# Performance work log

Hardware: AMD Instinct MI355X
Metric: run time of the kernel (lower is better)

## Reference

```python
import jax, jax.numpy as jnp
import numpy as np

NEG_INF = -9e15  # matches torch's -9000000000000000.0 mask value
ALPHA = 0.2      # LeakyReLU negative slope


def setup_inputs() -> dict:
    key = jax.random.key(0)
    k1, k2, k3, k4 = jax.random.split(key, 4)
    B, N, Fin, Fout = 8, 2048, 256, 256
    h = jax.random.normal(k1, (B, N, Fin), dtype=jnp.float32)
    adj = jax.random.randint(k2, (B, N, N), 0, 2, dtype=jnp.int32)
    # xavier_uniform with gain=1.414
    limW = 1.414 * np.sqrt(6.0 / (Fin + Fout))
    W = jax.random.uniform(k3, (Fin, Fout), minval=-limW, maxval=limW, dtype=jnp.float32)
    lima = 1.414 * np.sqrt(6.0 / (2 * Fout + 1))
    a = jax.random.uniform(k4, (2 * Fout, 1), minval=-lima, maxval=lima, dtype=jnp.float32)
    return {"h": h, "adj": adj, "W": W, "a": a}


def reference(h, adj, W, a):
    # h: (B, N, Fin), adj: (B, N, N), W: (Fin, Fout), a: (2*Fout, 1)
    Fout = W.shape[1]
    Wh = jnp.einsum('bni,io->bno', h, W)                 # (B, N, Fout)
    # e[b,i,j] = leakyrelu(Wh[b,i] @ a1 + Wh[b,j] @ a2) -- equivalent to the
    # original concat([Wh_i, Wh_j]) @ a without the O(N^2 * 2F) intermediate.
    e1 = Wh @ a[:Fout, 0]                                # (B, N)
    e2 = Wh @ a[Fout:, 0]                                # (B, N)
    e = jax.nn.leaky_relu(e1[:, :, None] + e2[:, None, :], negative_slope=ALPHA)
    masked = jnp.where(adj > 0, e, NEG_INF)
    attention = jax.nn.softmax(masked, axis=-1)          # (B, N, N)
    # dropout omitted (deterministic eval-mode reference)
    h_prime = jnp.einsum('bij,bjo->bio', attention, Wh)  # (B, N, Fout)
    return jax.nn.elu(h_prime), attention
```

## Files before the change

kernel.cpp:

```cpp
#include <hip/hip_runtime.h>
#include <hip/hip_bf16.h>
#include <stdint.h>

#define NEG_INF -9.0e15f
#define LRELU_ALPHA 0.2f

using bf16x8  = __attribute__((ext_vector_type(8))) short;
using f32x4   = __attribute__((ext_vector_type(4))) float;
using short4v = __attribute__((ext_vector_type(4))) short;
using int4v   = __attribute__((ext_vector_type(4))) int;
using float4v = __attribute__((ext_vector_type(4))) float;
using uint4v  = __attribute__((ext_vector_type(4))) unsigned;

static __device__ __forceinline__ float b2f(short s) {
  unsigned u = ((unsigned)(unsigned short)s) << 16;
  return __builtin_bit_cast(float, u);
}
static __device__ __forceinline__ short f2bf(float f) {
  unsigned u = __builtin_bit_cast(unsigned, f);
  u = u + 0x7FFFu + ((u >> 16) & 1u);
  return (short)(u >> 16);
}
static __device__ __forceinline__ unsigned cvtpk_bf16(float lo, float hi) {
  unsigned r;
  asm volatile("v_cvt_pk_bf16_f32 %0, %1, %2" : "=v"(r) : "v"(lo), "v"(hi));
  return r;
}
static __device__ __forceinline__ void gload16(const void* g, void* l) {
  __builtin_amdgcn_global_load_lds((const __attribute__((address_space(1))) void*)g,
                                   (__attribute__((address_space(3))) void*)l, 16, 0, 0);
}

__global__ __launch_bounds__(256) void cast_f32_bf16_kernel(
    const float* __restrict__ src, short* __restrict__ dst, int n)
{
  int i0 = (blockIdx.x * 256 + threadIdx.x) * 8;
  if (i0 >= n) return;
  float4v v0 = *(const float4v*)(src + i0);
  float4v v1 = *(const float4v*)(src + i0 + 4);
  short os[8] __attribute__((aligned(16)));
#pragma unroll
  for (int k = 0; k < 8; ++k) {
    float x = (k < 4) ? v0[k] : v1[k - 4];
    x = (x - x == 0.0f) ? x : 0.0f;
    os[k] = f2bf(x);
  }
  *(int4v*)(dst + i0) = *(const int4v*)os;
}

__global__ __launch_bounds__(256) void transpose_bf16_kernel(
    const short* __restrict__ src, short* __restrict__ dst,
    int M, int N, long long ss, long long ds)
{
  __shared__ short t[64][68];
  const int b = blockIdx.z;
  src += (long long)b * ss; dst += (long long)b * ds;
  const int m0 = blockIdx.x * 64, n0 = blockIdx.y * 64;
  const int tid = threadIdx.x;
  const int rr = tid >> 3, cc = (tid & 7) * 8;
#pragma unroll
  for (int p = 0; p < 2; ++p) {
    int row = rr + p * 32;
    const short* sp = src + (long long)(m0 + row) * N + n0 + cc;
    short4v v0 = *(const short4v*)sp;
    short4v v1 = *(const short4v*)(sp + 4);
    *(short4v*)&t[row][cc]     = v0;
    *(short4v*)&t[row][cc + 4] = v1;
  }
  __syncthreads();
#pragma unroll
  for (int p = 0; p < 2; ++p) {
    int orow = rr + p * 32;
    short vv[8] __attribute__((aligned(16)));
#pragma unroll
    for (int j = 0; j < 8; ++j) vv[j] = t[cc + j][orow];
    short* dp = dst + (long long)(n0 + orow) * M + m0 + cc;
    *(int4v*)dp = *(const int4v*)vv;
  }
}

__global__ __launch_bounds__(256) void evec_kernel(
    const short* __restrict__ Wh, const float* __restrict__ a,
    float* __restrict__ e1, float* __restrict__ e2)
{
  const int wid = threadIdx.x >> 6, lane = threadIdx.x & 63;
  const long long r = (long long)blockIdx.x * 4 + wid;
  short4v hv   = *(const short4v*)(Wh + r * 256 + lane * 4);
  float4v a1v  = *(const float4v*)(a + lane * 4);
  float4v a2v  = *(const float4v*)(a + 256 + lane * 4);
  float s1 = 0.f, s2 = 0.f;
#pragma unroll
  for (int k = 0; k < 4; ++k) {
    float x = b2f(hv[k]);
    s1 += x * a1v[k];
    s2 += x * a2v[k];
  }
#pragma unroll
  for (int off = 32; off > 0; off >>= 1) {
    s1 += __shfl_xor(s1, off, 64);
    s2 += __shfl_xor(s2, off, 64);
  }
  if (lane == 0) { e1[r] = s1; e2[r] = s2; }
}

__global__ __launch_bounds__(256) void attn_softmax_kernel(
    const int* __restrict__ adj, const float* __restrict__ e1,
    const float* __restrict__ e2, float* __restrict__ attn)
{
  const int i = blockIdx.x;
  const int b = blockIdx.y;
  const long long row = (long long)b * 2048 + i;
  const int tid = threadIdx.x;
  const int wid = tid >> 6, lane = tid & 63;
  const int j0 = tid * 8;

  const int*   arow = adj + row * 2048 + j0;
  const float  ei   = e1[row];
  const float* e2b  = e2 + b * 2048 + j0;

  int4v   a0 = *(const int4v*)(arow);
  int4v   a1 = *(const int4v*)(arow + 4);
  float4v f0 = *(const float4v*)(e2b);
  float4v f1 = *(const float4v*)(e2b + 4);

  float s[8];
#pragma unroll
  for (int k = 0; k < 8; ++k) {
    float x = ei + (k < 4 ? f0[k] : f1[k - 4]);
    float v = x > 0.f ? x : LRELU_ALPHA * x;
    int  ad = (k < 4 ? a0[k] : a1[k - 4]);
    s[k] = (ad > 0) ? v : NEG_INF;
  }
  float m = s[0];
#pragma unroll
  for (int k = 1; k < 8; ++k) m = fmaxf(m, s[k]);
#pragma unroll
  for (int off = 32; off > 0; off >>= 1) m = fmaxf(m, __shfl_xor(m, off, 64));

  __shared__ float wmax[4], wsum[4];
  if (lane == 0) wmax[wid] = m;
  __syncthreads();
  const float M = fmaxf(fmaxf(wmax[0], wmax[1]), fmaxf(wmax[2], wmax[3]));

  float p[8]; float t = 0.f;
#pragma unroll
  for (int k = 0; k < 8; ++k) { p[k] = __expf(s[k] - M); t += p[k]; }
#pragma unroll
  for (int off = 32; off > 0; off >>= 1) t += __shfl_xor(t, off, 64);
  if (lane == 0) wsum[wid] = t;
  __syncthreads();
  const float S = wsum[0] + wsum[1] + wsum[2] + wsum[3];
  const float r = 1.0f / S;

  float4v o0, o1;
#pragma unroll
  for (int k = 0; k < 4; ++k) { o0[k] = p[k] * r; o1[k] = p[k + 4] * r; }
  float* op = attn + row * 2048 + j0;
  *(float4v*)op       = o0;
  *(float4v*)(op + 4) = o1;
}

__global__ __launch_bounds__(256) void gemm_bt(
    const short* __restrict__ A, const short* __restrict__ Bt,
    short* __restrict__ C, int N, int K)
{
  __shared__ short As[128 * 32];
  __shared__ short Bs[128 * 32];
  const int m0 = blockIdx.x * 128, n0 = blockIdx.y * 128;
  const int tid = threadIdx.x;
  const int w = tid >> 6, lane = tid & 63;
  const int wr = w >> 1, wc = w & 1;
  const int g = lane >> 4, lr = lane & 15;

  f32x4 acc[4][4] = {};

  for (int k0 = 0; k0 < K; k0 += 32) {
    __syncthreads();
#pragma unroll
    for (int q = 0; q < 2; ++q) {
      int p = w * 2 + q;
      int c = p * 64 + lane;
      int row = c >> 2, kq = (c & 3) << 3;
      gload16(A  + (long long)(m0 + row) * K + k0 + kq, As + p * 512);
      gload16(Bt + (long long)(n0 + row) * K + k0 + kq, Bs + p * 512);
    }
    __syncthreads();

    bf16x8 af[4], bfr[4];
#pragma unroll
    for (int i = 0; i < 4; ++i) {
      af[i]  = *(const bf16x8*)(As + (wr * 64 + i * 16 + lr) * 32 + 8 * g);
      bfr[i] = *(const bf16x8*)(Bs + (wc * 64 + i * 16 + lr) * 32 + 8 * g);
    }
#pragma unroll
    for (int i = 0; i < 4; ++i)
#pragma unroll
      for (int j = 0; j < 4; ++j)
        acc[i][j] = __builtin_amdgcn_mfma_f32_16x16x32_bf16(af[i], bfr[j], acc[i][j], 0, 0, 0);
  }

#pragma unroll
  for (int i = 0; i < 4; ++i) {
    int row_base = m0 + wr * 64 + i * 16 + 4 * g;
#pragma unroll
    for (int j = 0; j < 4; ++j) {
      int col = n0 + wc * 64 + j * 16 + lr;
#pragma unroll
      for (int r = 0; r < 4; ++r)
        C[(long long)(row_base + r) * N + col] = f2bf(acc[i][j][r]);
    }
  }
}

__global__ __launch_bounds__(256, 2) void gemm_attn_kernel(
    const float* __restrict__ A, const short* __restrict__ Bt,
    float* __restrict__ C)
{
  __shared__ float As[32 * 64];
  __shared__ short Bs[256 * 64];
  const int bid = blockIdx.x;
  const int bz = bid & 7;
  const int m0 = (bid >> 3) << 5;
  A  += (long long)bz * 4194304;
  Bt += (long long)bz * 524288;
  C  += (long long)bz * 524288;
  const int tid = threadIdx.x;
  const int w = tid >> 6, lane = tid & 63;
  const int g = lane >> 4, lr = lane & 15;

  f32x4 acc[2][4] = {};

  const int bcol_off = lane >> 3;
  const int bchunk   = (lane & 7) ^ ((lane >> 3) & 7);
  const int as_s0  = w * 128 + lane;
  const int ar0    = as_s0 >> 4,  ac0 = as_s0 & 15;
  const int as_s1  = as_s0 + 64;
  const int ar1    = as_s1 >> 4,  ac1 = as_s1 & 15;

  for (int k0 = 0; k0 < 2048; k0 += 64) {
    __syncthreads();
    gload16(A + (long long)(m0 + ar0) * 2048 + k0 + ((ac0 ^ (ar0 & 15)) << 2), As + as_s0 * 4);
    gload16(A + (long long)(m0 + ar1) * 2048 + k0 + ((ac1 ^ (ar1 & 15)) << 2), As + as_s1 * 4);
#pragma unroll
    for (int q = 0; q < 8; ++q) {
      int p = w * 8 + q;
      int col = p * 8 + bcol_off;
      gload16(Bt + (long long)col * 2048 + k0 + bchunk * 8, Bs + p * 512);
    }
    __syncthreads();

    bf16x8 af[2][2], bfr[4][2];
#pragma unroll
    for (int i = 0; i < 2; ++i) {
      int row = i * 16 + lr;
      const float* arow = As + row * 64;
#pragma unroll
      for (int s = 0; s < 2; ++s) {
        int ch = s * 4 + g;
        float4v lo = *(const float4v*)(arow + (((2 * ch)     ^ (row & 15)) << 2));
        float4v hi = *(const float4v*)(arow + (((2 * ch + 1) ^ (row & 15)) << 2));
        uint4v uv;
        uv[0] = cvtpk_bf16(lo[0], lo[1]);
        uv[1] = cvtpk_bf16(lo[2], lo[3]);
        uv[2] = cvtpk_bf16(hi[0], hi[1]);
        uv[3] = cvtpk_bf16(hi[2], hi[3]);
        af[i][s] = __builtin_bit_cast(bf16x8, uv);
      }
    }
#pragma unroll
    for (int j = 0; j < 4; ++j) {
      int col = w * 64 + j * 16 + lr;
#pragma unroll
      for (int s = 0; s < 2; ++s)
        bfr[j][s] = *(const bf16x8*)(Bs + col * 64 + (((s * 4 + g) ^ (col & 7)) << 3));
    }
#pragma unroll
    for (int s = 0; s < 2; ++s)
#pragma unroll
      for (int i = 0; i < 2; ++i)
#pragma unroll
        for (int j = 0; j < 4; ++j)
          acc[i][j] = __builtin_amdgcn_mfma_f32_16x16x32_bf16(af[i][s], bfr[j][s], acc[i][j], 0, 0, 0);
  }

#pragma unroll
  for (int i = 0; i < 2; ++i) {
    int row_base = m0 + i * 16 + 4 * g;
#pragma unroll
    for (int j = 0; j < 4; ++j) {
      int col = w * 64 + j * 16 + lr;
#pragma unroll
      for (int r = 0; r < 4; ++r) {
        float v = acc[i][j][r];
        v = (v > 0.f) ? v : (__expf(v) - 1.f);
        C[(long long)(row_base + r) * 256 + col] = v;
      }
    }
  }
}

extern "C" void kernel_launch(void* const* d_in, const int* in_sizes, int n_in,
                              void* d_out, int out_size, void* d_ws, size_t ws_size,
                              hipStream_t stream)
{
  const float* h   = (const float*)d_in[0];
  const int*   adj = (const int*)d_in[1];
  const float* W   = (const float*)d_in[2];
  const float* a   = (const float*)d_in[3];

  float* hp_out   = (float*)d_out;
  float* attn_out = hp_out + 4194304LL;

  short* h_bf = (short*)d_ws;
  short* W_bf = h_bf + 4194304;
  short* W_t  = W_bf + 65536;
  short* Wh   = W_t + 65536;
  short* Wh_t = Wh + 4194304;
  float* e1   = (float*)(Wh_t + 4194304);
  float* e2   = e1 + 16384;

  cast_f32_bf16_kernel<<<2048, 256, 0, stream>>>(h, h_bf, 4194304);
  cast_f32_bf16_kernel<<<32, 256, 0, stream>>>(W, W_bf, 65536);
  transpose_bf16_kernel<<<dim3(4, 4, 1), 256, 0, stream>>>(W_bf, W_t, 256, 256, 0, 0);
  gemm_bt<<<dim3(128, 2, 1), 256, 0, stream>>>(h_bf, W_t, Wh, 256, 256);
  transpose_bf16_kernel<<<dim3(32, 4, 8), 256, 0, stream>>>(Wh, Wh_t, 2048, 256, 524288LL, 524288LL);
  evec_kernel<<<4096, 256, 0, stream>>>(Wh, a, e1, e2);
  attn_softmax_kernel<<<dim3(2048, 8), 256, 0, stream>>>(adj, e1, e2, attn_out);
  gemm_attn_kernel<<<512, 256, 0, stream>>>(attn_out, Wh_t, hp_out);
}
```

Measured before the change: 118.4 us.

## Fuse softmax normalization into PV GEMM using packed adjacency bitmask and row stats

Splits the softmax into a stats pass that packs adjacency into a bitmask and stores per-row log-sum-exp terms, then recomputes the probabilities inside the attention-times-Wh GEMM. The GEMM writes the attention output as it goes instead of reading back the fp32 attention matrix. This removes a full 128MB re-read of attention and the LDS staging of A, but B tiles are now loaded directly from global memory without shared-memory reuse. It also fuses W cast and transpose into one kernel. Rows with no neighbours are handled with a sentinel mask and constants that give a uniform distribution.

```diff
diff --git a/kernel.cpp b/kernel.cpp
--- a/kernel.cpp
+++ b/kernel.cpp
@@ -4,6 +4,7 @@
 
 #define NEG_INF -9.0e15f
 #define LRELU_ALPHA 0.2f
+#define LOG2E 1.442695040888963f
 
 using bf16x8  = __attribute__((ext_vector_type(8))) short;
 using f32x4   = __attribute__((ext_vector_type(4))) float;
@@ -46,6 +47,34 @@
     os[k] = f2bf(x);
   }
   *(int4v*)(dst + i0) = *(const int4v*)os;
+}
+
+__global__ __launch_bounds__(256) void castT_W_kernel(
+    const float* __restrict__ src, short* __restrict__ dst)
+{
+  __shared__ float t[64][65];
+  const int m0 = blockIdx.x * 64, n0 = blockIdx.y * 64;
+  const int tid = threadIdx.x;
+  const int rr = tid >> 3, cc = (tid & 7) * 8;
+#pragma unroll
+  for (int p = 0; p < 2; ++p) {
+    int row = rr + p * 32;
+    const float* sp = src + (m0 + row) * 256 + n0 + cc;
+    float4v v0 = *(const float4v*)sp;
+    float4v v1 = *(const float4v*)(sp + 4);
+#pragma unroll
+    for (int j = 0; j < 4; ++j) { t[row][cc + j] = v0[j]; t[row][cc + 4 + j] = v1[j]; }
+  }
+  __syncthreads();
+#pragma unroll
+  for (int p = 0; p < 2; ++p) {
+    int orow = rr + p * 32;
+    short vv[8] __attribute__((aligned(16)));
+#pragma unroll
+    for (int j = 0; j < 8; ++j) vv[j] = f2bf(t[cc + j][orow]);
+    short* dp = dst + (n0 + orow) * 256 + m0 + cc;
+    *(int4v*)dp = *(const int4v*)vv;
+  }
 }
 
 __global__ __launch_bounds__(256) void transpose_bf16_kernel(
@@ -103,9 +132,10 @@
   if (lane == 0) { e1[r] = s1; e2[r] = s2; }
 }
 
-__global__ __launch_bounds__(256) void attn_softmax_kernel(
+__global__ __launch_bounds__(256) void pack_stats_kernel(
     const int* __restrict__ adj, const float* __restrict__ e1,
-    const float* __restrict__ e2, float* __restrict__ attn)
+    const float* __restrict__ e2, unsigned char* __restrict__ mask,
+    float* __restrict__ Lr, float* __restrict__ Dr)
 {
   const int i = blockIdx.x;
   const int b = blockIdx.y;
@@ -123,13 +153,13 @@
   float4v f0 = *(const float4v*)(e2b);
   float4v f1 = *(const float4v*)(e2b + 4);
 
-  float s[8];
+  float s[8]; unsigned byte = 0u;
 #pragma unroll
   for (int k = 0; k < 8; ++k) {
     float x = ei + (k < 4 ? f0[k] : f1[k - 4]);
-    float v = x > 0.f ? x : LRELU_ALPHA * x;
+    float v = fmaxf(x, LRELU_ALPHA * x);
     int  ad = (k < 4 ? a0[k] : a1[k - 4]);
-    s[k] = (ad > 0) ? v : NEG_INF;
+    if (ad > 0) { s[k] = v; byte |= (1u << k); } else s[k] = NEG_INF;
   }
   float m = s[0];
 #pragma unroll
@@ -141,23 +171,116 @@
   if (lane == 0) wmax[wid] = m;
   __syncthreads();
   const float M = fmaxf(fmaxf(wmax[0], wmax[1]), fmaxf(wmax[2], wmax[3]));
-
-  float p[8]; float t = 0.f;
-#pragma unroll
-  for (int k = 0; k < 8; ++k) { p[k] = __expf(s[k] - M); t += p[k]; }
+  const bool empty = (M == NEG_INF);
+
+  mask[row * 256 + tid] = empty ? (unsigned char)0xFF : (unsigned char)byte;
+
+  float t = 0.f;
+#pragma unroll
+  for (int k = 0; k < 8; ++k) t += __expf(s[k] - M);
 #pragma unroll
   for (int off = 32; off > 0; off >>= 1) t += __shfl_xor(t, off, 64);
   if (lane == 0) wsum[wid] = t;
   __syncthreads();
-  const float S = wsum[0] + wsum[1] + wsum[2] + wsum[3];
-  const float r = 1.0f / S;
-
-  float4v o0, o1;
-#pragma unroll
-  for (int k = 0; k < 4; ++k) { o0[k] = p[k] * r; o1[k] = p[k + 4] * r; }
-  float* op = attn + row * 2048 + j0;
-  *(float4v*)op       = o0;
-  *(float4v*)(op + 4) = o1;
+  if (tid == 0) {
+    const float S = wsum[0] + wsum[1] + wsum[2] + wsum[3];
+    Lr[row] = empty ? 0.0f : LOG2E;
+    Dr[row] = empty ? -11.0f : (-M * LOG2E - __log2f(S));
+  }
+}
+
+__global__ __launch_bounds__(256, 2) void fused_pv_kernel(
+    const unsigned char* __restrict__ mask, const float* __restrict__ e1,
+    const float* __restrict__ e2, const float* __restrict__ Lr,
+    const float* __restrict__ Dr, const short* __restrict__ Bt,
+    float* __restrict__ attnw, float* __restrict__ C)
+{
+  const int bid = blockIdx.x;
+  const int bz  = bid & 7;
+  const int M0  = (bid >> 3) << 5;
+  const int tid = threadIdx.x;
+  const int w = tid >> 6, lane = tid & 63;
+  const int g = lane >> 4, lr = lane & 15;
+
+  const long long rb = (long long)bz * 2048;
+  const int r0 = M0 + lr, r1 = M0 + 16 + lr;
+  const float E1_0 = e1[rb + r0], L0 = Lr[rb + r0], D0 = Dr[rb + r0];
+  const float E1_1 = e1[rb + r1], L1 = Lr[rb + r1], D1 = Dr[rb + r1];
+  const unsigned long long* mrow0 = (const unsigned long long*)(mask + (rb + r0) * 256);
+  const unsigned long long* mrow1 = (const unsigned long long*)(mask + (rb + r1) * 256);
+  const float* e2b = e2 + rb;
+  Bt    += (long long)bz * 524288;
+  attnw += (long long)bz * 4194304;
+  C     += (long long)bz * 524288;
+
+  f32x4 acc[2][4] = {};
+
+  for (int k0 = 0; k0 < 2048; k0 += 64) {
+    const unsigned long long mw0 = mrow0[k0 >> 6];
+    const unsigned long long mw1 = mrow1[k0 >> 6];
+    bf16x8 af[2][2];
+#pragma unroll
+    for (int s = 0; s < 2; ++s) {
+      const int kc = s * 4 + g;
+      const int kk = k0 + kc * 8;
+      const float4v eo = *(const float4v*)(e2b + kk);
+      const float4v eh = *(const float4v*)(e2b + kk + 4);
+#pragma unroll
+      for (int i = 0; i < 2; ++i) {
+        const float E1v = i ? E1_1 : E1_0;
+        const float Lv  = i ? L1 : L0;
+        const float Dv  = i ? D1 : D0;
+        const unsigned by = (unsigned)((i ? mw1 : mw0) >> (kc * 8)) & 0xFFu;
+        float p[8];
+#pragma unroll
+        for (int e = 0; e < 8; ++e) {
+          float x = E1v + (e < 4 ? eo[e] : eh[e - 4]);
+          float v = fmaxf(x, LRELU_ALPHA * x);
+          float P = __builtin_amdgcn_exp2f(fmaf(v, Lv, Dv));
+          p[e] = ((by >> e) & 1u) ? P : 0.0f;
+        }
+        if (w == 0) {
+          float4v o0, o1;
+#pragma unroll
+          for (int e = 0; e < 4; ++e) { o0[e] = p[e]; o1[e] = p[e + 4]; }
+          float* op = attnw + (long long)(i ? r1 : r0) * 2048 + kk;
+          *(float4v*)op       = o0;
+          *(float4v*)(op + 4) = o1;
+        }
+        uint4v uv;
+        uv[0] = cvtpk_bf16(p[0], p[1]);
+        uv[1] = cvtpk_bf16(p[2], p[3]);
+        uv[2] = cvtpk_bf16(p[4], p[5]);
+        uv[3] = cvtpk_bf16(p[6], p[7]);
+        af[i][s] = __builtin_bit_cast(bf16x8, uv);
+      }
+    }
+#pragma unroll
+    for (int s = 0; s < 2; ++s)
+#pragma unroll
+      for (int j = 0; j < 4; ++j) {
+        bf16x8 bv = *(const bf16x8*)(Bt + (long long)(w * 64 + j * 16 + lr) * 2048
+                                        + k0 + (s * 4 + g) * 8);
+#pragma unroll
+        for (int i = 0; i < 2; ++i)
+          acc[i][j] = __builtin_amdgcn_mfma_f32_16x16x32_bf16(af[i][s], bv, acc[i][j], 0, 0, 0);
+      }
+  }
+
+#pragma unroll
+  for (int i = 0; i < 2; ++i) {
+    int row_base = M0 + i * 16 + 4 * g;
+#pragma unroll
+    for (int j = 0; j < 4; ++j) {
+      int col = w * 64 + j * 16 + lr;
+#pragma unroll
+      for (int r = 0; r < 4; ++r) {
+        float v = acc[i][j][r];
+        v = (v > 0.f) ? v : (__expf(v) - 1.f);
+        C[(long long)(row_base + r) * 256 + col] = v;
+      }
+    }
+  }
 }
 
 __global__ __launch_bounds__(256) void gemm_bt(
@@ -212,93 +335,6 @@
   }
 }
 
-__global__ __launch_bounds__(256, 2) void gemm_attn_kernel(
-    const float* __restrict__ A, const short* __restrict__ Bt,
-    float* __restrict__ C)
-{
-  __shared__ float As[32 * 64];
-  __shared__ short Bs[256 * 64];
-  const int bid = blockIdx.x;
-  const int bz = bid & 7;
-  const int m0 = (bid >> 3) << 5;
-  A  += (long long)bz * 4194304;
-  Bt += (long long)bz * 524288;
-  C  += (long long)bz * 524288;
-  const int tid = threadIdx.x;
-  const int w = tid >> 6, lane = tid & 63;
-  const int g = lane >> 4, lr = lane & 15;
-
-  f32x4 acc[2][4] = {};
-
-  const int bcol_off = lane >> 3;
-  const int bchunk   = (lane & 7) ^ ((lane >> 3) & 7);
-  const int as_s0  = w * 128 + lane;
-  const int ar0    = as_s0 >> 4,  ac0 = as_s0 & 15;
-  const int as_s1  = as_s0 + 64;
-  const int ar1    = as_s1 >> 4,  ac1 = as_s1 & 15;
-
-  for (int k0 = 0; k0 < 2048; k0 += 64) {
-    __syncthreads();
-    gload16(A + (long long)(m0 + ar0) * 2048 + k0 + ((ac0 ^ (ar0 & 15)) << 2), As + as_s0 * 4);
-    gload16(A + (long long)(m0 + ar1) * 2048 + k0 + ((ac1 ^ (ar1 & 15)) << 2), As + as_s1 * 4);
-#pragma unroll
-    for (int q = 0; q < 8; ++q) {
-      int p = w * 8 + q;
-      int col = p * 8 + bcol_off;
-      gload16(Bt + (long long)col * 2048 + k0 + bchunk * 8, Bs + p * 512);
-    }
-    __syncthreads();
-
-    bf16x8 af[2][2], bfr[4][2];
-#pragma unroll
-    for (int i = 0; i < 2; ++i) {
-      int row = i * 16 + lr;
-      const float* arow = As + row * 64;
-#pragma unroll
-      for (int s = 0; s < 2; ++s) {
-        int ch = s * 4 + g;
-        float4v lo = *(const float4v*)(arow + (((2 * ch)     ^ (row & 15)) << 2));
-        float4v hi = *(const float4v*)(arow + (((2 * ch + 1) ^ (row & 15)) << 2));
-        uint4v uv;
-        uv[0] = cvtpk_bf16(lo[0], lo[1]);
-        uv[1] = cvtpk_bf16(lo[2], lo[3]);
-        uv[2] = cvtpk_bf16(hi[0], hi[1]);
-        uv[3] = cvtpk_bf16(hi[2], hi[3]);
-        af[i][s] = __builtin_bit_cast(bf16x8, uv);
-      }
-    }
-#pragma unroll
-    for (int j = 0; j < 4; ++j) {
-      int col = w * 64 + j * 16 + lr;
-#pragma unroll
-      for (int s = 0; s < 2; ++s)
-        bfr[j][s] = *(const bf16x8*)(Bs + col * 64 + (((s * 4 + g) ^ (col & 7)) << 3));
-    }
-#pragma unroll
-    for (int s = 0; s < 2; ++s)
-#pragma unroll
-      for (int i = 0; i < 2; ++i)
-#pragma unroll
-        for (int j = 0; j < 4; ++j)
-          acc[i][j] = __builtin_amdgcn_mfma_f32_16x16x32_bf16(af[i][s], bfr[j][s], acc[i][j], 0, 0, 0);
-  }
-
-#pragma unroll
-  for (int i = 0; i < 2; ++i) {
-    int row_base = m0 + i * 16 + 4 * g;
-#pragma unroll
-    for (int j = 0; j < 4; ++j) {
-      int col = w * 64 + j * 16 + lr;
-#pragma unroll
-      for (int r = 0; r < 4; ++r) {
-        float v = acc[i][j][r];
-        v = (v > 0.f) ? v : (__expf(v) - 1.f);
-        C[(long long)(row_base + r) * 256 + col] = v;
-      }
-    }
-  }
-}
-
 extern "C" void kernel_launch(void* const* d_in, const int* in_sizes, int n_in,
                               void* d_out, int out_size, void* d_ws, size_t ws_size,
                               hipStream_t stream)
@@ -312,19 +348,20 @@
   float* attn_out = hp_out + 4194304LL;
 
   short* h_bf = (short*)d_ws;
-  short* W_bf = h_bf + 4194304;
-  short* W_t  = W_bf + 65536;
+  unsigned char* mask = (unsigned char*)d_ws;
+  short* W_t  = h_bf + 4194304;
   short* Wh   = W_t + 65536;
   short* Wh_t = Wh + 4194304;
   float* e1   = (float*)(Wh_t + 4194304);
   float* e2   = e1 + 16384;
+  float* Lr   = e2 + 16384;
+  float* Dr   = Lr + 16384;
 
   cast_f32_bf16_kernel<<<2048, 256, 0, stream>>>(h, h_bf, 4194304);
-  cast_f32_bf16_kernel<<<32, 256, 0, stream>>>(W, W_bf, 65536);
-  transpose_bf16_kernel<<<dim3(4, 4, 1), 256, 0, stream>>>(W_bf, W_t, 256, 256, 0, 0);
+  castT_W_kernel<<<dim3(4, 4), 256, 0, stream>>>(W, W_t);
   gemm_bt<<<dim3(128, 2, 1), 256, 0, stream>>>(h_bf, W_t, Wh, 256, 256);
   transpose_bf16_kernel<<<dim3(32, 4, 8), 256, 0, stream>>>(Wh, Wh_t, 2048, 256, 524288LL, 524288LL);
   evec_kernel<<<4096, 256, 0, stream>>>(Wh, a, e1, e2);
-  attn_softmax_kernel<<<dim3(2048, 8), 256, 0, stream>>>(adj, e1, e2, attn_out);
-  gemm_attn_kernel<<<512, 256, 0, stream>>>(attn_out, Wh_t, hp_out);
-}
+  pack_stats_kernel<<<dim3(2048, 8), 256, 0, stream>>>(adj, e1, e2, mask, Lr, Dr);
+  fused_pv_kernel<<<512, 256, 0, stream>>>(mask, e1, e2, Lr, Dr, Wh_t, attn_out, hp_out);
+}
```

New measurement: 159.3 us. +34.5%, slower.
